# Kernel tuning notes

Hardware: AMD Instinct MI355X
Metric: run time of the kernel (lower is better)

Reference implementation:

```python
import jax, jax.numpy as jnp
import numpy as np

B, T, I, H, O, L = 128, 512, 64, 256, 2, 2


def _gru_layer(x_seq, w_ih, w_hh, b_ih, b_hh):
    # x_seq: [B, T, in], w_ih: [3H, in], w_hh: [3H, H], biases: [3H]
    # PyTorch gate order: r, z, n
    xg = jnp.einsum('bti,gi->btg', x_seq, w_ih) + b_ih  # [B, T, 3H]
    h0 = jnp.zeros((x_seq.shape[0], w_hh.shape[1]), x_seq.dtype)

    def step(h, xg_t):
        hg = h @ w_hh.T + b_hh  # [B, 3H]
        xr, xz, xn = jnp.split(xg_t, 3, axis=-1)
        hr, hz, hn = jnp.split(hg, 3, axis=-1)
        r = jax.nn.sigmoid(xr + hr)
        z = jax.nn.sigmoid(xz + hz)
        n = jnp.tanh(xn + r * hn)
        h_new = (1.0 - z) * n + z * h
        return h_new, h_new

    _, hs = jax.lax.scan(step, h0, jnp.swapaxes(xg, 0, 1))  # [T, B, H]
    return jnp.swapaxes(hs, 0, 1)  # [B, T, H]


def setup_inputs() -> dict:
    key = jax.random.key(0)
    ks = jax.random.split(key, 12)
    s_ih0 = 1.0 / np.sqrt(H)
    inp = {
        'x': jax.random.normal(ks[0], (B, T, I), jnp.float32),
        'w_ih0': jax.random.uniform(ks[1], (3 * H, I), jnp.float32, -s_ih0, s_ih0),
        'w_hh0': jax.random.uniform(ks[2], (3 * H, H), jnp.float32, -s_ih0, s_ih0),
        'b_ih0': jax.random.uniform(ks[3], (3 * H,), jnp.float32, -s_ih0, s_ih0),
        'b_hh0': jax.random.uniform(ks[4], (3 * H,), jnp.float32, -s_ih0, s_ih0),
        'w_ih1': jax.random.uniform(ks[5], (3 * H, H), jnp.float32, -s_ih0, s_ih0),
        'w_hh1': jax.random.uniform(ks[6], (3 * H, H), jnp.float32, -s_ih0, s_ih0),
        'b_ih1': jax.random.uniform(ks[7], (3 * H,), jnp.float32, -s_ih0, s_ih0),
        'b_hh1': jax.random.uniform(ks[8], (3 * H,), jnp.float32, -s_ih0, s_ih0),
        'fc_w': jax.random.uniform(ks[9], (O, H), jnp.float32, -s_ih0, s_ih0),
        'fc_b': jax.random.uniform(ks[10], (O,), jnp.float32, -s_ih0, s_ih0),
    }
    return inp


def reference(x, w_ih0, w_hh0, b_ih0, b_hh0, w_ih1, w_hh1, b_ih1, b_hh1, fc_w, fc_b):
    h1 = _gru_layer(x, w_ih0, w_hh0, b_ih0, b_hh0)   # [B, T, H]
    h2 = _gru_layer(h1, w_ih1, w_hh1, b_ih1, b_hh1)  # [B, T, H]
    last = jax.nn.relu(h2[:, -1])                     # [B, H]
    return last @ fc_w.T + fc_b                       # [B, O]
```

## Files before the change

### kernel.cpp

```cpp
#include <hip/hip_runtime.h>


namespace {
constexpr int kB = 128, kT = 512, kI = 64, kH = 256, kBH = kB * kH;
constexpr int NG = 8, GW = 32, RPG = 16, NWG = 256, NT = 512;

constexpr int SRS = 36;
constexpr int SKS = 16 * SRS + 4;
constexpr int O_S0 = 0;
constexpr int O_S1 = O_S0 + 8 * SKS;
constexpr int O_X  = O_S1 + 8 * SKS;
constexpr int O_PB = O_X + RPG * 68;
constexpr int PBN  = 4 * 16 * 36;
constexpr int LDSF = O_PB + PBN;

constexpr int FS = 16;
}

using ull = unsigned long long;

__device__ __forceinline__ float sigf(float v) { return 1.0f / (1.0f + expf(-v)); }
__device__ __forceinline__ float dot4(const float4 a, const float4 b) {
  return a.x * b.x + a.y * b.y + a.z * b.z + a.w * b.w;
}
__device__ __forceinline__ float red8(float v) {
  v += __shfl_xor(v, 8);
  v += __shfl_xor(v, 16);
  v += __shfl_xor(v, 32);
  return v;
}
#define F4(p) (*(const float4*)(p))

__global__ __launch_bounds__(NT, 2) void gru_persistent(
    const float* __restrict__ x,
    const float* __restrict__ wih0, const float* __restrict__ whh0,
    const float* __restrict__ bih0, const float* __restrict__ bhh0,
    const float* __restrict__ wih1, const float* __restrict__ whh1,
    const float* __restrict__ bih1, const float* __restrict__ bhh1,
    const float* __restrict__ fcw, const float* __restrict__ fcb,
    unsigned* __restrict__ h0w,
    unsigned* __restrict__ h1w,
    unsigned* __restrict__ sd,
    float* __restrict__ out)
{
  __shared__ float lds[LDSF];

  const int bid = blockIdx.x;
  const int g   = bid >> 5;
  const int wg  = bid & (GW - 1);
  const int tid = threadIdx.x;
  const int r0  = g * RPG;
  const int j0  = wg * 8;

  const int wave = tid >> 6;
  const int lane = tid & 63;
  const int lay  = wave >> 2;
  const int fam  = (wave >> 1) & 1;
  const int rh   = wave & 1;
  const int ju   = lane & 7;
  const int ks   = lane >> 3;
  const int jg   = j0 + ju;

  for (int i = tid; i < PBN; i += NT) lds[O_PB + i] = 0.f;

  float4 wr0[8], wr1[8], wr2[8];
  if (lay == 0) {
    if (fam == 0) {
#define L0F0(wrg, gg) { \
      const float* wi = wih0 + (size_t)((gg) * kH + jg) * kI + ks * 8;   \
      const float* wh = whh0 + (size_t)((gg) * kH + jg) * kH + ks * 32;  \
      wrg[0] = F4(wi); wrg[1] = F4(wi + 4);                              \
      wrg[2] = F4(wh); wrg[3] = F4(wh + 4); wrg[4] = F4(wh + 8); }
      L0F0(wr0, 0) L0F0(wr1, 1) L0F0(wr2, 2)
    } else {
#define L0F1(wrg, gg) { \
      const float* wh = whh0 + (size_t)((gg) * kH + jg) * kH + ks * 32 + 12; \
      wrg[0] = F4(wh); wrg[1] = F4(wh + 4); wrg[2] = F4(wh + 8);             \
      wrg[3] = F4(wh + 12); wrg[4] = F4(wh + 16); }
      L0F1(wr0, 0) L0F1(wr1, 1) L0F1(wr2, 2)
    }
  } else {
    const float* ws = fam ? whh1 : wih1;
#define L1W(wrg, gg) { \
    const float* wp = ws + (size_t)((gg) * kH + jg) * kH + ks * 32;          \
    wrg[0] = F4(wp);      wrg[1] = F4(wp + 4);  wrg[2] = F4(wp + 8);         \
    wrg[3] = F4(wp + 12); wrg[4] = F4(wp + 16); wrg[5] = F4(wp + 20);        \
    wrg[6] = F4(wp + 24); wrg[7] = F4(wp + 28); }
    L1W(wr0, 0) L1W(wr1, 1) L1W(wr2, 2)
  }

  float fb_r = 0.f, fb_z = 0.f, fb_ni = 0.f, fb_nh = 0.f;
  if (tid < 256) {
    const int layf = tid >> 7, uf = tid & 7, jf = j0 + uf;
    const float* bi = layf ? bih1 : bih0;
    const float* bh = layf ? bhh1 : bhh0;
    fb_r  = bi[jf] + bh[jf];
    fb_z  = bi[kH + jf] + bh[kH + jf];
    fb_ni = bi[2 * kH + jf];
    fb_nh = bh[2 * kH + jf];
  }

  int RO[4], K2[4];
  #pragma unroll
  for (int p = 0; p < 4; ++p) {
    const int i = tid + p * NT;
    RO[p] = i >> 7; K2[p] = i & 127;
  }

  __syncthreads();

  for (int s = 0; s <= kT; ++s) {
    const int slot0 = (s + 2) % 3;
    const int slot1 = (s + 1) % 3;
    const unsigned e0 = (unsigned)(s & 3);
    const unsigned e1 = (unsigned)((s - 1) & 3);

    if (s < kT && tid < 256) {
      const int ro = tid >> 4, c4 = (tid & 15) * 4;
      *(float4*)(lds + O_X + ro * 68 + c4) =
          F4(x + (size_t)(r0 + ro) * kT * kI + (size_t)s * kI + c4);
    }
    if (s >= 2 && tid >= 480) {
      const unsigned* f = sd + (unsigned)((g << 5) + (tid - 480)) * FS;
      while (__hip_atomic_load(f, __ATOMIC_RELAXED, __HIP_MEMORY_SCOPE_AGENT)
             < (unsigned)(s - 1)) { }
    }

    ull v0[4], v1[4];
    {
      const ull* A0[4]; const ull* A1[4];
      #pragma unroll
      for (int p = 0; p < 4; ++p) {
        A0[p] = (const ull*)(h0w + (size_t)slot0 * kBH +
                             (size_t)(r0 + RO[p]) * kH) + K2[p];
        A1[p] = (const ull*)(h1w + (size_t)slot1 * kBH +
                             (size_t)(r0 + RO[p]) * kH) + K2[p];
      }
      for (;;) {
        #pragma unroll
        for (int p = 0; p < 4; ++p)
          v0[p] = __hip_atomic_load(A0[p], __ATOMIC_RELAXED,
                                    __HIP_MEMORY_SCOPE_AGENT);
        if (s >= 1) {
          #pragma unroll
          for (int p = 0; p < 4; ++p)
            v1[p] = __hip_atomic_load(A1[p], __ATOMIC_RELAXED,
                                      __HIP_MEMORY_SCOPE_AGENT);
        }
        unsigned bad = 0;
        #pragma unroll
        for (int p = 0; p < 4; ++p)
          bad |= ((unsigned)v0[p] ^ e0) | ((unsigned)(v0[p] >> 32) ^ e0);
        if (s >= 1) {
          #pragma unroll
          for (int p = 0; p < 4; ++p)
            bad |= ((unsigned)v1[p] ^ e1) | ((unsigned)(v1[p] >> 32) ^ e1);
        }
        if (!(bad & 3u)) break;
      }
    }
    #pragma unroll
    for (int p = 0; p < 4; ++p) {
      const int ksg = K2[p] >> 4, off = (K2[p] * 2) & 31, ro = RO[p];
      float2 f0; __builtin_memcpy(&f0, &v0[p], 8);
      *(float2*)(lds + O_S0 + ksg * SKS + ro * SRS + off) = f0;
      if (s >= 1) {
        float2 f1; __builtin_memcpy(&f1, &v1[p], 8);
        *(float2*)(lds + O_S1 + ksg * SKS + ro * SRS + off) = f1;
      }
    }
    __syncthreads();
    if (tid == 0) {
      __hip_atomic_store(sd + (unsigned)bid * FS, (unsigned)(s + 1),
                         __ATOMIC_RELAXED, __HIP_MEMORY_SCOPE_AGENT);
    }

    const bool wact = lay ? (s >= 1) : (s < kT);
    if (wact) {
      float prr[8], pzz[8], pni[8], pnh[8];
      #pragma unroll
      for (int r = 0; r < 8; ++r) {
        const int ro = rh * 8 + r;
        float pr = 0.f, pz = 0.f, pxi = 0.f, pxh = 0.f;
        if (lay == 0) {
          if (fam == 0) {
            const float* ax = lds + O_X + ro * 68 + ks * 8;
            const float4 x0 = F4(ax), x1 = F4(ax + 4);
            pr  += dot4(x0, wr0[0]) + dot4(x1, wr0[1]);
            pz  += dot4(x0, wr1[0]) + dot4(x1, wr1[1]);
            pxi += dot4(x0, wr2[0]) + dot4(x1, wr2[1]);
            const float* ah = lds + O_S0 + ks * SKS + ro * SRS;
            #pragma unroll
            for (int i = 0; i < 3; ++i) {
              const float4 hv = F4(ah + i * 4);
              pr  += dot4(hv, wr0[2 + i]);
              pz  += dot4(hv, wr1[2 + i]);
              pxh += dot4(hv, wr2[2 + i]);
            }
          } else {
            const float* ah = lds + O_S0 + ks * SKS + ro * SRS + 12;
            #pragma unroll
            for (int i = 0; i < 5; ++i) {
              const float4 hv = F4(ah + i * 4);
              pr  += dot4(hv, wr0[i]);
              pz  += dot4(hv, wr1[i]);
              pxh += dot4(hv, wr2[i]);
            }
          }
        } else {
          const float* aa = lds + (fam ? O_S1 : O_S0) + ks * SKS + ro * SRS;
          #pragma unroll
          for (int i = 0; i < 8; ++i) {
            const float4 av = F4(aa + i * 4);
            pr += dot4(av, wr0[i]);
            pz += dot4(av, wr1[i]);
            if (fam) pxh += dot4(av, wr2[i]);
            else     pxi += dot4(av, wr2[i]);
          }
        }
        prr[r] = pr; pzz[r] = pz; pni[r] = pxi; pnh[r] = pxh;
      }
      #pragma unroll
      for (int r = 0; r < 8; ++r) { prr[r] = red8(prr[r]); pzz[r] = red8(pzz[r]); }
      if (lay == 0 && fam == 0) {
        #pragma unroll
        for (int r = 0; r < 8; ++r) { pni[r] = red8(pni[r]); pnh[r] = red8(pnh[r]); }
      } else if (fam == 0) {
        #pragma unroll
        for (int r = 0; r < 8; ++r) pni[r] = red8(pni[r]);
      } else {
        #pragma unroll
        for (int r = 0; r < 8; ++r) pnh[r] = red8(pnh[r]);
      }
      if (ks == 0) {
        #pragma unroll
        for (int r = 0; r < 8; ++r) {
          float* pb = lds + O_PB + ((wave >> 1) * 16 + rh * 8 + r) * SRS + ju;
          pb[0] = prr[r]; pb[8] = pzz[r];
          if (lay == 0 && fam == 0) { pb[16] = pni[r]; pb[24] = pnh[r]; }
          else if (fam == 0)          pb[16] = pni[r];
          else                        pb[24] = pnh[r];
        }
      }
    }
    __syncthreads();

    if (tid < 256) {
      const int layf = tid >> 7;
      const bool act = layf ? (s >= 1) : (s < kT);
      if (act) {
        const int rof = (tid >> 3) & 15, uf = tid & 7, jf = j0 + uf;
        const float* p0 = lds + O_PB + ((layf * 2) * 16 + rof) * SRS + uf;
        const float* p1 = p0 + 16 * SRS;
        const float rr = sigf(p0[0] + p1[0] + fb_r);
        const float zz = sigf(p0[8] + p1[8] + fb_z);
        const float nn = tanhf(p0[16] + p1[16] + fb_ni +
                               rr * (p0[24] + p1[24] + fb_nh));
        const float hp = lds[(layf ? O_S1 : O_S0) +
                             (jf >> 5) * SKS + rof * SRS + (jf & 31)];
        const float hv = (1.f - zz) * nn + zz * hp;
        const int slot = layf ? ((s - 1) % 3) : (s % 3);
        const unsigned tag = layf ? (unsigned)(s & 3) : (unsigned)((s + 1) & 3);
        const unsigned bits = (__float_as_uint(hv) & ~3u) | tag;
        unsigned* hw = (layf ? h1w : h0w) + (size_t)slot * kBH +
                       (size_t)(r0 + rof) * kH + jf;
        __hip_atomic_store(hw, bits, __ATOMIC_RELAXED,
                           __HIP_MEMORY_SCOPE_AGENT);
      }
    }
    __syncthreads();
  }

  if (wg == 0 && tid < 256) {
    const int rv = tid >> 4, o = (tid >> 3) & 1, kseg = tid & 7;
    const unsigned* hf = h1w + (size_t)((kT - 1) % 3) * kBH +
                         (size_t)(r0 + rv) * kH;
    const float* wfc = fcw + (size_t)o * kH;
    float acc = 0.f;
    for (int k = kseg * 32; k < kseg * 32 + 32; ++k) {
      unsigned b;
      do {
        b = __hip_atomic_load(hf + k, __ATOMIC_RELAXED,
                              __HIP_MEMORY_SCOPE_AGENT);
      } while ((b & 3u) != (unsigned)(kT & 3));
      acc += fmaxf(__uint_as_float(b), 0.f) * wfc[k];
    }
    acc += __shfl_xor(acc, 1);
    acc += __shfl_xor(acc, 2);
    acc += __shfl_xor(acc, 4);
    if (kseg == 0) out[(r0 + rv) * 2 + o] = acc + fcb[o];
  }
}

extern "C" void kernel_launch(void* const* d_in, const int* in_sizes, int n_in,
                              void* d_out, int out_size, void* d_ws, size_t ws_size,
                              hipStream_t stream) {
  const float* x    = (const float*)d_in[0];
  const float* wih0 = (const float*)d_in[1];
  const float* whh0 = (const float*)d_in[2];
  const float* bih0 = (const float*)d_in[3];
  const float* bhh0 = (const float*)d_in[4];
  const float* wih1 = (const float*)d_in[5];
  const float* whh1 = (const float*)d_in[6];
  const float* bih1 = (const float*)d_in[7];
  const float* bhh1 = (const float*)d_in[8];
  const float* fcw  = (const float*)d_in[9];
  const float* fcb  = (const float*)d_in[10];

  unsigned* h0w = (unsigned*)d_ws;
  unsigned* h1w = h0w + 3 * kBH;
  unsigned* sd  = h1w + 3 * kBH;
  float* out = (float*)d_out;

  hipMemsetAsync(d_ws, 0,
                 (size_t)(6 * kBH) * sizeof(unsigned) +
                 (size_t)NWG * FS * sizeof(unsigned), stream);

  gru_persistent<<<NWG, NT, 0, stream>>>(
      x, wih0, whh0, bih0, bhh0, wih1, whh1, bih1, bhh1,
      fcw, fcb, h0w, h1w, sd, out);
}
```

Before: 3.470 ms.

## Double-buffer LDS, defer gate finish into next step, drop flag barrier

Measured after the change: 4.083 ms. 17.7% more time.

```diff
diff --git a/kernel.cpp b/kernel.cpp
--- a/kernel.cpp
+++ b/kernel.cpp
@@ -3,7 +3,7 @@
 
 namespace {
 constexpr int kB = 128, kT = 512, kI = 64, kH = 256, kBH = kB * kH;
-constexpr int NG = 8, GW = 32, RPG = 16, NWG = 256, NT = 512;
+constexpr int RPG = 16, NWG = 256, NT = 512;
 
 constexpr int SRS = 36;
 constexpr int SKS = 16 * SRS + 4;
@@ -13,11 +13,10 @@
 constexpr int O_PB = O_X + RPG * 68;
 constexpr int PBN  = 4 * 16 * 36;
 constexpr int LDSF = O_PB + PBN;
-
-constexpr int FS = 16;
 }
 
 using ull = unsigned long long;
+using u32 = unsigned;
 
 __device__ __forceinline__ float sigf(float v) { return 1.0f / (1.0f + expf(-v)); }
 __device__ __forceinline__ float dot4(const float4 a, const float4 b) {
@@ -30,6 +29,8 @@
   return v;
 }
 #define F4(p) (*(const float4*)(p))
+#define AL(p)    __hip_atomic_load((p), __ATOMIC_RELAXED, __HIP_MEMORY_SCOPE_AGENT)
+#define AS(p, v) __hip_atomic_store((p), (v), __ATOMIC_RELAXED, __HIP_MEMORY_SCOPE_AGENT)
 
 __global__ __launch_bounds__(NT, 2) void gru_persistent(
     const float* __restrict__ x,
@@ -38,22 +39,20 @@
     const float* __restrict__ wih1, const float* __restrict__ whh1,
     const float* __restrict__ bih1, const float* __restrict__ bhh1,
     const float* __restrict__ fcw, const float* __restrict__ fcb,
-    unsigned* __restrict__ h0w,
-    unsigned* __restrict__ h1w,
-    unsigned* __restrict__ sd,
+    u32* __restrict__ h0w,
+    u32* __restrict__ h1w,
     float* __restrict__ out)
 {
-  __shared__ float lds[LDSF];
+  __shared__ float lds[2 * LDSF];
 
   const int bid = blockIdx.x;
   const int g   = bid >> 5;
-  const int wg  = bid & (GW - 1);
+  const int wg  = bid & 31;
   const int tid = threadIdx.x;
   const int r0  = g * RPG;
   const int j0  = wg * 8;
 
-  const int wave = tid >> 6;
-  const int lane = tid & 63;
+  const int wave = tid >> 6, lane = tid & 63;
   const int lay  = wave >> 2;
   const int fam  = (wave >> 1) & 1;
   const int rh   = wave & 1;
@@ -61,7 +60,10 @@
   const int ks   = lane >> 3;
   const int jg   = j0 + ju;
 
-  for (int i = tid; i < PBN; i += NT) lds[O_PB + i] = 0.f;
+  for (int i = tid; i < PBN; i += NT) {
+    lds[O_PB + i] = 0.f;
+    lds[LDSF + O_PB + i] = 0.f;
+  }
 
   float4 wr0[8], wr1[8], wr2[8];
   if (lay == 0) {
@@ -89,15 +91,15 @@
     L1W(wr0, 0) L1W(wr1, 1) L1W(wr2, 2)
   }
 
-  float fb_r = 0.f, fb_z = 0.f, fb_ni = 0.f, fb_nh = 0.f;
+  float fb_r = 0.f, fb_z = 0.f, fn_i = 0.f, fn_h = 0.f;
   if (tid < 256) {
     const int layf = tid >> 7, uf = tid & 7, jf = j0 + uf;
     const float* bi = layf ? bih1 : bih0;
     const float* bh = layf ? bhh1 : bhh0;
-    fb_r  = bi[jf] + bh[jf];
-    fb_z  = bi[kH + jf] + bh[kH + jf];
-    fb_ni = bi[2 * kH + jf];
-    fb_nh = bh[2 * kH + jf];
+    fb_r = bi[jf] + bh[jf];
+    fb_z = bi[kH + jf] + bh[kH + jf];
+    fn_i = bi[2 * kH + jf];
+    fn_h = bh[2 * kH + jf];
   }
 
   int RO[4], K2[4];
@@ -107,73 +109,101 @@
     RO[p] = i >> 7; K2[p] = i & 127;
   }
 
+  auto finish_u = [&](int u, const float* Lp) {
+    if (tid < 256) {
+      const int layf = tid >> 7;
+      const bool act = layf ? (u >= 1) : (u < kT);
+      if (act) {
+        const int rof = (tid >> 3) & 15, uf = tid & 7, jf = j0 + uf;
+        const float* p0 = Lp + O_PB + ((layf * 2) * 16 + rof) * SRS + uf;
+        const float* p1 = p0 + 16 * SRS;
+        const float rr = sigf(p0[0] + p1[0] + fb_r);
+        const float zz = sigf(p0[8] + p1[8] + fb_z);
+        const float nn = tanhf(p0[16] + p1[16] + fn_i +
+                               rr * (p0[24] + p1[24] + fn_h));
+        const float hp = Lp[(layf ? O_S1 : O_S0) +
+                            (jf >> 5) * SKS + rof * SRS + (jf & 31)];
+        const float hv = (1.f - zz) * nn + zz * hp;
+        const int slot = layf ? ((u - 1) % 3) : (u % 3);
+        const u32 tag = layf ? (u32)(u & 3) : (u32)((u + 1) & 3);
+        const u32 bits = (__float_as_uint(hv) & ~3u) | tag;
+        u32* hw = (layf ? h1w : h0w) + (size_t)slot * kBH +
+                  (size_t)(r0 + rof) * kH + jf;
+        AS(hw, bits);
+      }
+    }
+  };
+
   __syncthreads();
 
   for (int s = 0; s <= kT; ++s) {
+    float* Lc = lds + (s & 1) * LDSF;
+    const float* Lp = lds + ((s & 1) ^ 1) * LDSF;
+
     const int slot0 = (s + 2) % 3;
     const int slot1 = (s + 1) % 3;
-    const unsigned e0 = (unsigned)(s & 3);
-    const unsigned e1 = (unsigned)((s - 1) & 3);
-
+    const u32 e0 = (u32)(s & 3);
+    const u32 e1 = (u32)((s - 1) & 3);
+
+    const ull* A0[4]; const ull* A1[4];
+    ull v0[4], v1[4];
+    #pragma unroll
+    for (int p = 0; p < 4; ++p) {
+      A0[p] = (const ull*)(h0w + (size_t)slot0 * kBH +
+                           (size_t)(r0 + RO[p]) * kH) + K2[p];
+      v0[p] = AL(A0[p]);
+    }
+    if (s >= 1) {
+      #pragma unroll
+      for (int p = 0; p < 4; ++p) {
+        A1[p] = (const ull*)(h1w + (size_t)slot1 * kBH +
+                             (size_t)(r0 + RO[p]) * kH) + K2[p];
+        v1[p] = AL(A1[p]);
+      }
+    }
+    float4 xv = {};
     if (s < kT && tid < 256) {
       const int ro = tid >> 4, c4 = (tid & 15) * 4;
-      *(float4*)(lds + O_X + ro * 68 + c4) =
-          F4(x + (size_t)(r0 + ro) * kT * kI + (size_t)s * kI + c4);
-    }
-    if (s >= 2 && tid >= 480) {
-      const unsigned* f = sd + (unsigned)((g << 5) + (tid - 480)) * FS;
-      while (__hip_atomic_load(f, __ATOMIC_RELAXED, __HIP_MEMORY_SCOPE_AGENT)
-             < (unsigned)(s - 1)) { }
-    }
-
-    ull v0[4], v1[4];
-    {
-      const ull* A0[4]; const ull* A1[4];
-      #pragma unroll
-      for (int p = 0; p < 4; ++p) {
-        A0[p] = (const ull*)(h0w + (size_t)slot0 * kBH +
-                             (size_t)(r0 + RO[p]) * kH) + K2[p];
-        A1[p] = (const ull*)(h1w + (size_t)slot1 * kBH +
-                             (size_t)(r0 + RO[p]) * kH) + K2[p];
-      }
-      for (;;) {
+      xv = F4(x + (size_t)(r0 + ro) * kT * kI + (size_t)s * kI + c4);
+    }
+
+    if (s >= 1) finish_u(s - 1, Lp);
+    asm volatile("" ::: "memory");
+
+    for (;;) {
+      u32 bad = 0;
+      #pragma unroll
+      for (int p = 0; p < 4; ++p)
+        bad |= ((u32)v0[p] ^ e0) | ((u32)(v0[p] >> 32) ^ e0);
+      if (s >= 1) {
         #pragma unroll
         for (int p = 0; p < 4; ++p)
-          v0[p] = __hip_atomic_load(A0[p], __ATOMIC_RELAXED,
-                                    __HIP_MEMORY_SCOPE_AGENT);
-        if (s >= 1) {
-          #pragma unroll
-          for (int p = 0; p < 4; ++p)
-            v1[p] = __hip_atomic_load(A1[p], __ATOMIC_RELAXED,
-                                      __HIP_MEMORY_SCOPE_AGENT);
-        }
-        unsigned bad = 0;
-        #pragma unroll
-        for (int p = 0; p < 4; ++p)
-          bad |= ((unsigned)v0[p] ^ e0) | ((unsigned)(v0[p] >> 32) ^ e0);
-        if (s >= 1) {
-          #pragma unroll
-          for (int p = 0; p < 4; ++p)
-            bad |= ((unsigned)v1[p] ^ e1) | ((unsigned)(v1[p] >> 32) ^ e1);
-        }
-        if (!(bad & 3u)) break;
+          bad |= ((u32)v1[p] ^ e1) | ((u32)(v1[p] >> 32) ^ e1);
+      }
+      if (!(bad & 3u)) break;
+      __builtin_amdgcn_s_sleep(1);
+      #pragma unroll
+      for (int p = 0; p < 4; ++p) v0[p] = AL(A0[p]);
+      if (s >= 1) {
+        #pragma unroll
+        for (int p = 0; p < 4; ++p) v1[p] = AL(A1[p]);
       }
     }
     #pragma unroll
     for (int p = 0; p < 4; ++p) {
       const int ksg = K2[p] >> 4, off = (K2[p] * 2) & 31, ro = RO[p];
       float2 f0; __builtin_memcpy(&f0, &v0[p], 8);
-      *(float2*)(lds + O_S0 + ksg * SKS + ro * SRS + off) = f0;
+      *(float2*)(Lc + O_S0 + ksg * SKS + ro * SRS + off) = f0;
       if (s >= 1) {
         float2 f1; __builtin_memcpy(&f1, &v1[p], 8);
-        *(float2*)(lds + O_S1 + ksg * SKS + ro * SRS + off) = f1;
-      }
+        *(float2*)(Lc + O_S1 + ksg * SKS + ro * SRS + off) = f1;
+      }
+    }
+    if (s < kT && tid < 256) {
+      const int ro = tid >> 4, c4 = (tid & 15) * 4;
+      *(float4*)(Lc + O_X + ro * 68 + c4) = xv;
     }
     __syncthreads();
-    if (tid == 0) {
-      __hip_atomic_store(sd + (unsigned)bid * FS, (unsigned)(s + 1),
-                         __ATOMIC_RELAXED, __HIP_MEMORY_SCOPE_AGENT);
-    }
 
     const bool wact = lay ? (s >= 1) : (s < kT);
     if (wact) {
@@ -184,12 +214,12 @@
         float pr = 0.f, pz = 0.f, pxi = 0.f, pxh = 0.f;
         if (lay == 0) {
           if (fam == 0) {
-            const float* ax = lds + O_X + ro * 68 + ks * 8;
+            const float* ax = Lc + O_X + ro * 68 + ks * 8;
             const float4 x0 = F4(ax), x1 = F4(ax + 4);
             pr  += dot4(x0, wr0[0]) + dot4(x1, wr0[1]);
             pz  += dot4(x0, wr1[0]) + dot4(x1, wr1[1]);
             pxi += dot4(x0, wr2[0]) + dot4(x1, wr2[1]);
-            const float* ah = lds + O_S0 + ks * SKS + ro * SRS;
+            const float* ah = Lc + O_S0 + ks * SKS + ro * SRS;
             #pragma unroll
             for (int i = 0; i < 3; ++i) {
               const float4 hv = F4(ah + i * 4);
@@ -198,7 +228,7 @@
               pxh += dot4(hv, wr2[2 + i]);
             }
           } else {
-            const float* ah = lds + O_S0 + ks * SKS + ro * SRS + 12;
+            const float* ah = Lc + O_S0 + ks * SKS + ro * SRS + 12;
             #pragma unroll
             for (int i = 0; i < 5; ++i) {
               const float4 hv = F4(ah + i * 4);
@@ -208,7 +238,7 @@
             }
           }
         } else {
-          const float* aa = lds + (fam ? O_S1 : O_S0) + ks * SKS + ro * SRS;
+          const float* aa = Lc + (fam ? O_S1 : O_S0) + ks * SKS + ro * SRS;
           #pragma unroll
           for (int i = 0; i < 8; ++i) {
             const float4 av = F4(aa + i * 4);
@@ -235,7 +265,7 @@
       if (ks == 0) {
         #pragma unroll
         for (int r = 0; r < 8; ++r) {
-          float* pb = lds + O_PB + ((wave >> 1) * 16 + rh * 8 + r) * SRS + ju;
+          float* pb = Lc + O_PB + ((wave >> 1) * 16 + rh * 8 + r) * SRS + ju;
           pb[0] = prr[r]; pb[8] = pzz[r];
           if (lay == 0 && fam == 0) { pb[16] = pni[r]; pb[24] = pnh[r]; }
           else if (fam == 0)          pb[16] = pni[r];
@@ -244,45 +274,20 @@
       }
     }
     __syncthreads();
-
-    if (tid < 256) {
-      const int layf = tid >> 7;
-      const bool act = layf ? (s >= 1) : (s < kT);
-      if (act) {
-        const int rof = (tid >> 3) & 15, uf = tid & 7, jf = j0 + uf;
-        const float* p0 = lds + O_PB + ((layf * 2) * 16 + rof) * SRS + uf;
-        const float* p1 = p0 + 16 * SRS;
-        const float rr = sigf(p0[0] + p1[0] + fb_r);
-        const float zz = sigf(p0[8] + p1[8] + fb_z);
-        const float nn = tanhf(p0[16] + p1[16] + fb_ni +
-                               rr * (p0[24] + p1[24] + fb_nh));
-        const float hp = lds[(layf ? O_S1 : O_S0) +
-                             (jf >> 5) * SKS + rof * SRS + (jf & 31)];
-        const float hv = (1.f - zz) * nn + zz * hp;
-        const int slot = layf ? ((s - 1) % 3) : (s % 3);
-        const unsigned tag = layf ? (unsigned)(s & 3) : (unsigned)((s + 1) & 3);
-        const unsigned bits = (__float_as_uint(hv) & ~3u) | tag;
-        unsigned* hw = (layf ? h1w : h0w) + (size_t)slot * kBH +
-                       (size_t)(r0 + rof) * kH + jf;
-        __hip_atomic_store(hw, bits, __ATOMIC_RELAXED,
-                           __HIP_MEMORY_SCOPE_AGENT);
-      }
-    }
-    __syncthreads();
-  }
+  }
+
+  finish_u(kT, lds + (kT & 1) * LDSF);
 
   if (wg == 0 && tid < 256) {
     const int rv = tid >> 4, o = (tid >> 3) & 1, kseg = tid & 7;
-    const unsigned* hf = h1w + (size_t)((kT - 1) % 3) * kBH +
-                         (size_t)(r0 + rv) * kH;
+    const u32* hf = h1w + (size_t)((kT - 1) % 3) * kBH + (size_t)(r0 + rv) * kH;
     const float* wfc = fcw + (size_t)o * kH;
     float acc = 0.f;
     for (int k = kseg * 32; k < kseg * 32 + 32; ++k) {
-      unsigned b;
+      u32 b;
       do {
-        b = __hip_atomic_load(hf + k, __ATOMIC_RELAXED,
-                              __HIP_MEMORY_SCOPE_AGENT);
-      } while ((b & 3u) != (unsigned)(kT & 3));
+        b = AL(hf + k);
+      } while ((b & 3u) != (u32)(kT & 3));
       acc += fmaxf(__uint_as_float(b), 0.f) * wfc[k];
     }
     acc += __shfl_xor(acc, 1);
@@ -307,16 +312,13 @@
   const float* fcw  = (const float*)d_in[9];
   const float* fcb  = (const float*)d_in[10];
 
-  unsigned* h0w = (unsigned*)d_ws;
-  unsigned* h1w = h0w + 3 * kBH;
-  unsigned* sd  = h1w + 3 * kBH;
+  u32* h0w = (u32*)d_ws;
+  u32* h1w = h0w + 3 * kBH;
   float* out = (float*)d_out;
 
-  hipMemsetAsync(d_ws, 0,
-                 (size_t)(6 * kBH) * sizeof(unsigned) +
-                 (size_t)NWG * FS * sizeof(unsigned), stream);
+  hipMemsetAsync(d_ws, 0, (size_t)(6 * kBH) * sizeof(u32), stream);
 
   gru_persistent<<<NWG, NT, 0, stream>>>(
       x, wih0, whh0, bih0, bhh0, wih1, whh1, bih1, bhh1,
-      fcw, fcb, h0w, h1w, sd, out);
-}
+      fcw, fcb, h0w, h1w, out);
+}
```
